# Kernel optimization log

Measured on AMD Instinct MI355X. Metric: run time of the kernel, lower is better.

Reference implementation:

```python
import jax, jax.numpy as jnp
import numpy as np

NUM_HEADS = 4
NUM_EXPERTS = 8
TOP_K = 2
AUX_W = 0.1


def setup_inputs() -> dict:
    key = jax.random.key(0)
    ks = jax.random.split(key, 16)
    B, W, C, T = 32, 64, 27, 2000
    E_EEG, H, S = 200, 256, 768
    D2 = 2 * H  # MoE input/hidden dim = 512
    s = 0.02

    def p(k, shape):
        return (jax.random.normal(k, shape, jnp.float32) * s)

    z = lambda *shape: jnp.zeros(shape, jnp.float32)
    return {
        "eeg_windows": jax.random.normal(ks[0], (B, W, C, T), jnp.float32),
        "padding_mask": jnp.zeros((B, W), bool),
        "smiles_emb": jax.random.normal(ks[1], (B, S), jnp.float32),
        # window encoder (linear stand-in): flatten (C*T) -> E_EEG
        "enc_W": p(ks[2], (C * T, E_EEG)), "enc_b": z(E_EEG),
        # aggregator (masked-mean + linear stand-in): E_EEG -> H
        "agg_W": p(ks[3], (E_EEG, H)), "agg_b": z(H),
        # smiles projection
        "smiles_W": p(ks[4], (S, H)), "smiles_b": z(H),
        # cross attention
        "Wq": p(ks[5], (H, H)), "bq": z(H),
        "Wk": p(ks[6], (H, H)), "bk": z(H),
        "Wv": p(ks[7], (H, H)), "bv": z(H),
        "Wo": p(ks[8], (H, H)), "bo": z(H),
        # MoE gate + experts
        "gate_W": p(ks[9], (D2, NUM_EXPERTS)), "gate_b": z(NUM_EXPERTS),
        "exp_W1": p(ks[10], (NUM_EXPERTS, D2, D2)), "exp_b1": z(NUM_EXPERTS, D2),
        "exp_W2": p(ks[11], (NUM_EXPERTS, D2, H)), "exp_b2": z(NUM_EXPERTS, H),
        # classifier
        "ln_g": jnp.ones((H,), jnp.float32), "ln_b": z(H),
        "cls_W": p(ks[12], (H, 2)), "cls_b": z(2),
    }


def reference(eeg_windows, padding_mask, smiles_emb, enc_W, enc_b, agg_W, agg_b,
              smiles_W, smiles_b, Wq, bq, Wk, bk, Wv, bv, Wo, bo,
              gate_W, gate_b, exp_W1, exp_b1, exp_W2, exp_b2,
              ln_g, ln_b, cls_W, cls_b):
    B, W, C, T = eeg_windows.shape
    H = agg_W.shape[1]
    dh = H // NUM_HEADS

    # --- window encoding (stand-in linear encoder) ---
    wemb = eeg_windows.reshape(B, W, C * T) @ enc_W + enc_b  # (B, W, E_EEG)

    # --- aggregator: masked mean pool over windows, then project ---
    valid = (~padding_mask).astype(wemb.dtype)[..., None]      # (B, W, 1)
    pooled = (wemb * valid).sum(1) / jnp.maximum(valid.sum(1), 1.0)
    eeg_emb = pooled @ agg_W + agg_b                           # (B, H)

    smiles_proj = smiles_emb @ smiles_W + smiles_b             # (B, H)

    # --- cross attention (single query token over single kv token) ---
    q = (eeg_emb @ Wq + bq).reshape(B, NUM_HEADS, dh)
    k = (smiles_proj @ Wk + bk).reshape(B, NUM_HEADS, dh)
    v = (smiles_proj @ Wv + bv).reshape(B, NUM_HEADS, dh)
    scores = (q * k).sum(-1, keepdims=True) / jnp.sqrt(jnp.float32(dh))
    attn = jnp.exp(scores - scores)  # softmax over a single key == 1
    attended = (attn * v).reshape(B, H) @ Wo + bo              # (B, H)

    fused = jnp.concatenate([attended, smiles_proj], axis=-1)  # (B, 2H)

    # --- sparse MoE: dense experts, top-k gate, gather, combine ---
    gate_probs = jax.nn.softmax(fused @ gate_W + gate_b, axis=-1)  # (B, E)
    topk_p, topk_i = jax.lax.top_k(gate_probs, TOP_K)
    topk_p = topk_p / topk_p.sum(-1, keepdims=True)
    h1 = jax.nn.gelu(jnp.einsum('bd,edh->beh', fused, exp_W1) + exp_b1,
                     approximate=False)
    expert_out = jnp.einsum('beh,eho->beo', h1, exp_W2) + exp_b2   # (B, E, H)
    sel = jnp.take_along_axis(expert_out, topk_i[:, :, None], axis=1)
    moe_out = (sel * topk_p[..., None]).sum(1)                     # (B, H)

    usage = gate_probs.mean(0)
    uniform = jnp.ones_like(usage) / usage.shape[-1]
    aux = (usage * jnp.log(uniform) - jnp.log(usage) * uniform).sum()

    # --- classifier: LayerNorm + Linear ---
    mu = moe_out.mean(-1, keepdims=True)
    var = moe_out.var(-1, keepdims=True)
    xn = (moe_out - mu) / jnp.sqrt(var + 1e-5)
    logits = (xn * ln_g + ln_b) @ cls_W + cls_b                    # (B, 2)
    return logits, aux * AUX_W
```

## Files before the change

kernel.cpp:

```cpp
#include <hip/hip_runtime.h>
#include <math.h>

#define HD 256
#define SD 768
#define D2 512
#define NE 8
#define NB 32
#define NBLK 256
#define NTHR 256
#define SFP 516

typedef float f32x4 __attribute__((ext_vector_type(4)));
typedef unsigned u32x4 __attribute__((ext_vector_type(4)));

__device__ __forceinline__ float gelu_exact(float x) {
    return 0.5f * x * (1.0f + erff(x * 0.70710678118654752f));
}

__device__ __forceinline__ void cstf(float* p, float v) {
    __hip_atomic_store(p, v, __ATOMIC_RELAXED, __HIP_MEMORY_SCOPE_AGENT);
}
__device__ __forceinline__ float cldf(const float* p) {
    return __hip_atomic_load(p, __ATOMIC_RELAXED, __HIP_MEMORY_SCOPE_AGENT);
}
__device__ __forceinline__ void csti(int* p, int v) {
    __hip_atomic_store(p, v, __ATOMIC_RELAXED, __HIP_MEMORY_SCOPE_AGENT);
}
__device__ __forceinline__ int cldi(const int* p) {
    return __hip_atomic_load(p, __ATOMIC_RELAXED, __HIP_MEMORY_SCOPE_AGENT);
}

__device__ __forceinline__ void stage16k(const float* __restrict__ gsrc,
                                         float* __restrict__ lds, int t)
{
    const f32x4* src = (const f32x4*)gsrc;
    f32x4 r[16];
    #pragma unroll
    for (int j = 0; j < 16; ++j) {
        const f32x4* p = src + (t + j * 256);
        asm volatile("global_load_dwordx4 %0, %1, off sc0 sc1"
                     : "=v"(r[j]) : "v"(p));
    }
    asm volatile("s_waitcnt vmcnt(0)" ::: "memory");
    __builtin_amdgcn_sched_barrier(0);
    #pragma unroll
    for (int j = 0; j < 16; ++j) {
        int q = t + j * 256;
        *(f32x4*)&lds[(q >> 7) * SFP + (q & 127) * 4] = r[j];
    }
}

__device__ __forceinline__ void post_slot(unsigned* slots, unsigned tok) {
    __syncthreads();
    if (threadIdx.x == 0)
        __hip_atomic_store(slots + blockIdx.x, tok, __ATOMIC_RELAXED,
                           __HIP_MEMORY_SCOPE_AGENT);
}

__device__ __forceinline__ void finish_full(const unsigned* slots,
                                            unsigned* gen, unsigned tok) {
    const int t = threadIdx.x;
    if (blockIdx.x == 0) {
        if (t < 64) {
            const u32x4* p = (const u32x4*)slots + t;
            for (;;) {
                u32x4 v;
                asm volatile("global_load_dwordx4 %0, %1, off sc0 sc1\n\t"
                             "s_waitcnt vmcnt(0)"
                             : "=&v"(v) : "v"(p) : "memory");
                bool ok = (v[0] == tok) & (v[1] == tok) &
                          (v[2] == tok) & (v[3] == tok);
                if (__ballot(ok) == ~0ull) break;
                __builtin_amdgcn_s_sleep(1);
            }
            if (t == 0)
                __hip_atomic_store(gen, tok, __ATOMIC_RELAXED,
                                   __HIP_MEMORY_SCOPE_AGENT);
        }
    } else {
        if (t == 0) {
            while (__hip_atomic_load(gen, __ATOMIC_RELAXED,
                                     __HIP_MEMORY_SCOPE_AGENT) != tok)
                __builtin_amdgcn_s_sleep(1);
        }
    }
    __builtin_amdgcn_fence(__ATOMIC_ACQUIRE, "workgroup");
    __syncthreads();
}

__device__ __forceinline__ void wait_subset(const unsigned* slots, int nq,
                                            unsigned tok) {
    if ((int)threadIdx.x < nq) {
        const u32x4* p = (const u32x4*)slots + threadIdx.x;
        for (;;) {
            u32x4 v;
            asm volatile("global_load_dwordx4 %0, %1, off sc0 sc1\n\t"
                         "s_waitcnt vmcnt(0)"
                         : "=&v"(v) : "v"(p) : "memory");
            if ((v[0] == tok) & (v[1] == tok) & (v[2] == tok) & (v[3] == tok))
                break;
            __builtin_amdgcn_s_sleep(2);
        }
    }
    __builtin_amdgcn_fence(__ATOMIC_ACQUIRE, "workgroup");
    __syncthreads();
}

__device__ __forceinline__ void wait_two_experts(const unsigned* slots,
                                                 int ea, int eb, unsigned tok) {
    if (threadIdx.x < 8) {
        int es = (threadIdx.x < 4) ? ea : eb;
        const u32x4* p = (const u32x4*)slots + es * 4 + (threadIdx.x & 3);
        for (;;) {
            u32x4 v;
            asm volatile("global_load_dwordx4 %0, %1, off sc0 sc1\n\t"
                         "s_waitcnt vmcnt(0)"
                         : "=&v"(v) : "v"(p) : "memory");
            if ((v[0] == tok) & (v[1] == tok) & (v[2] == tok) & (v[3] == tok))
                break;
            __builtin_amdgcn_s_sleep(2);
        }
    }
    __builtin_amdgcn_fence(__ATOMIC_ACQUIRE, "workgroup");
    __syncthreads();
}

#define S_F     0
#define S_W     16512
#define S_R2    (16512 + 8192)
#define S_RED   (16512 + 8192 + 4096)
#define S_SMALL (16512 + 8192 + 4096 + 256)
#define SMEM_F  (16512 + 8192 + 4096 + 256 + 16)

__global__ __launch_bounds__(256) void fused_all(
    const float* __restrict__ smiles,
    const float* __restrict__ sW, const float* __restrict__ sb,
    const float* __restrict__ Wv, const float* __restrict__ bv,
    const float* __restrict__ Wo, const float* __restrict__ bo,
    const float* __restrict__ gW, const float* __restrict__ gb,
    const float* __restrict__ W1, const float* __restrict__ b1,
    const float* __restrict__ W2, const float* __restrict__ b2,
    const float* __restrict__ lng, const float* __restrict__ lnb,
    const float* __restrict__ clsW, const float* __restrict__ clsb,
    float* __restrict__ proj, float* __restrict__ fused,
    float* __restrict__ probs, float* __restrict__ pn,
    int* __restrict__ sel, float* __restrict__ h1,
    float* __restrict__ eo,
    unsigned* __restrict__ slot0, unsigned* __restrict__ slot1,
    unsigned* __restrict__ slot2, unsigned* __restrict__ slot3,
    unsigned* __restrict__ gen, unsigned* __restrict__ LC,
    float* __restrict__ out)
{
    __shared__ __align__(16) float smem[SMEM_F];
    __shared__ unsigned s_lc;
    const int bid = blockIdx.x, t = threadIdx.x;

    if (t == 0)
        s_lc = __hip_atomic_load(LC, __ATOMIC_RELAXED, __HIP_MEMORY_SCOPE_AGENT);
    __syncthreads();
    const unsigned tb = s_lc * 2654435761u;

    {
        int r = bid >> 3, sl = bid & 7;
        float* s_in = smem + S_F;
        float* s_red = smem + S_RED;
        const float* srow = smiles + (size_t)r * SD;
        for (int i = t; i < SD / 4; i += NTHR)
            ((float4*)s_in)[i] = ((const float4*)srow)[i];
        __syncthreads();
        int c = t & 31, kq = t >> 5;
        float acc = 0.f;
        const float* wp = sW + (size_t)(kq * 96) * HD + sl * 32 + c;
        #pragma unroll 8
        for (int k = 0; k < 96; ++k)
            acc = fmaf(s_in[kq * 96 + k], wp[(size_t)k * HD], acc);
        s_red[t] = acc;
        __syncthreads();
        if (t < 32) {
            float s = 0.f;
            #pragma unroll
            for (int q = 0; q < 8; ++q) s += s_red[q * 32 + t];
            int col = sl * 32 + t;
            s += sb[col];
            cstf(proj + r * HD + col, s);
            cstf(fused + (size_t)r * 2 * HD + HD + col, s);
        }
    }
    post_slot(slot0, tb + 1u);

    if (bid < NB) {
        wait_subset(slot0 + bid * 8, 2, tb + 1u);
        int b = bid;
        float* s_p   = smem + S_F;
        float* s_v   = smem + S_F + 256;
        float* s_f2  = smem + S_F + 512;
        float* s_acc = smem + S_R2;
        float* s_red = smem + S_RED;
        float* s_gate = smem + S_SMALL;
        s_p[t] = cldf(proj + b * HD + t);
        __syncthreads();
        int ks = t >> 6, cg = t & 63;

        f32x4 av = {0.f, 0.f, 0.f, 0.f};
        #pragma unroll 16
        for (int kk = 0; kk < 64; ++kk) {
            int k = ks * 64 + kk;
            f32x4 w = *(const f32x4*)(Wv + (size_t)k * HD + cg * 4);
            av += s_p[k] * w;
        }
        *(f32x4*)&s_acc[ks * 256 + cg * 4] = av;
        __syncthreads();
        s_v[t] = s_acc[t] + s_acc[256 + t] + s_acc[512 + t] + s_acc[768 + t]
               + bv[t];
        __syncthreads();

        f32x4 ao = {0.f, 0.f, 0.f, 0.f};
        #pragma unroll 16
        for (int kk = 0; kk < 64; ++kk) {
            int k = ks * 64 + kk;
            f32x4 w = *(const f32x4*)(Wo + (size_t)k * HD + cg * 4);
            ao += s_v[k] * w;
        }
        *(f32x4*)&s_acc[ks * 256 + cg * 4] = ao;
        __syncthreads();
        float att = s_acc[t] + s_acc[256 + t] + s_acc[512 + t] + s_acc[768 + t]
                  + bo[t];
        s_f2[t] = att;
        s_f2[HD + t] = s_p[t];
        cstf(fused + (size_t)b * 2 * HD + t, att);
        __syncthreads();

        int e = t & 7, ch = t >> 3;
        float gp = 0.f;
        #pragma unroll
        for (int j = 0; j < 16; ++j) {
            int d = ch * 16 + j;
            gp = fmaf(s_f2[d], gW[d * NE + e], gp);
        }
        s_red[t] = gp;
        __syncthreads();
        for (int off = 128; off >= 8; off >>= 1) {
            if (t < off) s_red[t] += s_red[t + off];
            __syncthreads();
        }
        if (t < NE) s_gate[t] = s_red[t] + gb[t];
        __syncthreads();
        if (t == 0) {
            float m = s_gate[0];
            for (int i = 1; i < NE; ++i) m = fmaxf(m, s_gate[i]);
            float ex[NE], ssum = 0.f;
            for (int i = 0; i < NE; ++i) { ex[i] = expf(s_gate[i] - m); ssum += ex[i]; }
            float pr[NE];
            for (int i = 0; i < NE; ++i) { pr[i] = ex[i] / ssum; cstf(probs + b * NE + i, pr[i]); }
            int i1 = 0;
            for (int i = 1; i < NE; ++i) if (pr[i] > pr[i1]) i1 = i;
            int i2 = (i1 == 0) ? 1 : 0;
            for (int i = 0; i < NE; ++i) if (i != i1 && pr[i] > pr[i2]) i2 = i;
            float p1 = pr[i1], p2 = pr[i2], s12 = p1 + p2;
            csti(sel + b * 2 + 0, i1);
            csti(sel + b * 2 + 1, i2);
            cstf(pn + b * 2 + 0, p1 / s12);
            cstf(pn + b * 2 + 1, p2 / s12);
        }
    }
    post_slot(slot1, tb + 2u);

    {
        int e = bid >> 5, ct = bid & 31;
        float* s_w = smem + S_W;
        const float* Wb = W1 + (size_t)e * D2 * D2 + ct * 16;
        #pragma unroll
        for (int j = 0; j < 8; ++j) {
            int q = t + j * 256;
            int k = q >> 2, c4 = (q & 3) * 4;
            *(float4*)&s_w[k * 16 + c4] = *(const float4*)(Wb + (size_t)k * D2 + c4);
        }
    }
    finish_full(slot1, gen + 0, tb + 2u);

    {
        int e = bid >> 5, ct = bid & 31;
        float* s_f  = smem + S_F;
        float* s_w  = smem + S_W;
        float* s_r2 = smem + S_R2;
        stage16k(fused, s_f, t);
        __syncthreads();
        int ks = t >> 5, l = t & 31;
        int rg = l >> 2, c4g = l & 3;
        const float* wb = s_w + c4g * 4;
        int k0 = ks * 64;
        f32x4 a0 = {0.f,0.f,0.f,0.f}, a1 = a0, a2 = a0, a3 = a0;
        #pragma unroll 2
        for (int kq = 0; kq < 16; ++kq) {
            int k = k0 + kq * 4;
            f32x4 w0 = *(const f32x4*)&wb[(k + 0) * 16];
            f32x4 w1 = *(const f32x4*)&wb[(k + 1) * 16];
            f32x4 w2 = *(const f32x4*)&wb[(k + 2) * 16];
            f32x4 w3 = *(const f32x4*)&wb[(k + 3) * 16];
            f32x4 f0 = *(const f32x4*)&s_f[(rg     ) * SFP + k];
            f32x4 f1 = *(const f32x4*)&s_f[(rg +  8) * SFP + k];
            f32x4 f2 = *(const f32x4*)&s_f[(rg + 16) * SFP + k];
            f32x4 f3 = *(const f32x4*)&s_f[(rg + 24) * SFP + k];
            a0 += f0[0]*w0 + f0[1]*w1 + f0[2]*w2 + f0[3]*w3;
            a1 += f1[0]*w0 + f1[1]*w1 + f1[2]*w2 + f1[3]*w3;
            a2 += f2[0]*w0 + f2[1]*w1 + f2[2]*w2 + f2[3]*w3;
            a3 += f3[0]*w0 + f3[1]*w1 + f3[2]*w2 + f3[3]*w3;
        }
        *(f32x4*)&s_r2[ks * 512 + (rg     ) * 16 + c4g * 4] = a0;
        *(f32x4*)&s_r2[ks * 512 + (rg +  8) * 16 + c4g * 4] = a1;
        *(f32x4*)&s_r2[ks * 512 + (rg + 16) * 16 + c4g * 4] = a2;
        *(f32x4*)&s_r2[ks * 512 + (rg + 24) * 16 + c4g * 4] = a3;
        __syncthreads();
        #pragma unroll
        for (int o = 0; o < 2; ++o) {
            int outi = t * 2 + o;
            float s = 0.f;
            #pragma unroll
            for (int p = 0; p < 8; ++p) s += s_r2[p * 512 + outi];
            int r = outi >> 4, cl = outi & 15;
            int col = ct * 16 + cl;
            cstf(h1 + ((size_t)e * NB + r) * D2 + col,
                 gelu_exact(s + b1[e * D2 + col]));
        }
    }
    post_slot(slot2, tb + 3u);
    if (bid >= 128) return;

    {
        int e = bid >> 4, ct = bid & 15;
        float* s_w = smem + S_W;
        const float* Wb = W2 + (size_t)e * D2 * HD + ct * 16;
        #pragma unroll
        for (int j = 0; j < 8; ++j) {
            int q = t + j * 256;
            int k = q >> 2, c4 = (q & 3) * 4;
            *(float4*)&s_w[k * 16 + c4] = *(const float4*)(Wb + (size_t)k * HD + c4);
        }
    }
    {
        int e = bid >> 4;
        wait_subset(slot2 + e * 32, 8, tb + 3u);
    }

    {
        int e = bid >> 4, ct = bid & 15;
        float* s_f  = smem + S_F;
        float* s_w  = smem + S_W;
        float* s_r2 = smem + S_R2;
        stage16k(h1 + (size_t)e * NB * D2, s_f, t);
        __syncthreads();
        int ks = t >> 5, l = t & 31;
        int rg = l >> 2, c4g = l & 3;
        const float* wb = s_w + c4g * 4;
        int k0 = ks * 64;
        f32x4 a0 = {0.f,0.f,0.f,0.f}, a1 = a0, a2 = a0, a3 = a0;
        #pragma unroll 2
        for (int kq = 0; kq < 16; ++kq) {
            int k = k0 + kq * 4;
            f32x4 w0 = *(const f32x4*)&wb[(k + 0) * 16];
            f32x4 w1 = *(const f32x4*)&wb[(k + 1) * 16];
            f32x4 w2 = *(const f32x4*)&wb[(k + 2) * 16];
            f32x4 w3 = *(const f32x4*)&wb[(k + 3) * 16];
            f32x4 f0 = *(const f32x4*)&s_f[(rg     ) * SFP + k];
            f32x4 f1 = *(const f32x4*)&s_f[(rg +  8) * SFP + k];
            f32x4 f2 = *(const f32x4*)&s_f[(rg + 16) * SFP + k];
            f32x4 f3 = *(const f32x4*)&s_f[(rg + 24) * SFP + k];
            a0 += f0[0]*w0 + f0[1]*w1 + f0[2]*w2 + f0[3]*w3;
            a1 += f1[0]*w0 + f1[1]*w1 + f1[2]*w2 + f1[3]*w3;
            a2 += f2[0]*w0 + f2[1]*w1 + f2[2]*w2 + f2[3]*w3;
            a3 += f3[0]*w0 + f3[1]*w1 + f3[2]*w2 + f3[3]*w3;
        }
        *(f32x4*)&s_r2[ks * 512 + (rg     ) * 16 + c4g * 4] = a0;
        *(f32x4*)&s_r2[ks * 512 + (rg +  8) * 16 + c4g * 4] = a1;
        *(f32x4*)&s_r2[ks * 512 + (rg + 16) * 16 + c4g * 4] = a2;
        *(f32x4*)&s_r2[ks * 512 + (rg + 24) * 16 + c4g * 4] = a3;
        __syncthreads();
        #pragma unroll
        for (int o = 0; o < 2; ++o) {
            int outi = t * 2 + o;
            float s = 0.f;
            #pragma unroll
            for (int p = 0; p < 8; ++p) s += s_r2[p * 512 + outi];
            int r = outi >> 4, cl = outi & 15;
            int col = ct * 16 + cl;
            cstf(eo + ((size_t)e * NB + r) * HD + col, s + b2[e * HD + col]);
        }
    }
    post_slot(slot3, tb + 4u);
    if (bid >= NB) return;

    {
        int b = bid;
        float* s_red = smem + S_RED;
        float* s_stats = smem + S_SMALL;
        int e0 = cldi(sel + b * 2 + 0), e1 = cldi(sel + b * 2 + 1);
        float p0 = cldf(pn + b * 2 + 0), p1 = cldf(pn + b * 2 + 1);

        wait_two_experts(slot3, e0, e1, tb + 4u);

        float moe = p0 * cldf(eo + ((size_t)e0 * NB + b) * HD + t)
                  + p1 * cldf(eo + ((size_t)e1 * NB + b) * HD + t);

        s_red[t] = moe; __syncthreads();
        for (int off = 128; off > 0; off >>= 1) {
            if (t < off) s_red[t] += s_red[t + off];
            __syncthreads();
        }
        if (t == 0) s_stats[0] = s_red[0] * (1.f / HD);
        __syncthreads();
        float mu = s_stats[0];
        float d = moe - mu;

        s_red[t] = d * d; __syncthreads();
        for (int off = 128; off > 0; off >>= 1) {
            if (t < off) s_red[t] += s_red[t + off];
            __syncthreads();
        }
        if (t == 0) s_stats[1] = s_red[0] * (1.f / HD);
        __syncthreads();

        float xn = d * rsqrtf(s_stats[1] + 1e-5f);
        float y = fmaf(xn, lng[t], lnb[t]);

        s_red[t] = y * clsW[t * 2 + 0]; __syncthreads();
        for (int off = 128; off > 0; off >>= 1) {
            if (t < off) s_red[t] += s_red[t + off];
            __syncthreads();
        }
        if (t == 0) s_stats[2] = s_red[0] + clsb[0];
        __syncthreads();

        s_red[t] = y * clsW[t * 2 + 1]; __syncthreads();
        for (int off = 128; off > 0; off >>= 1) {
            if (t < off) s_red[t] += s_red[t + off];
            __syncthreads();
        }
        if (t == 0) {
            out[b * 2 + 0] = s_stats[2];
            out[b * 2 + 1] = s_red[0] + clsb[1];
        }

        if (bid == 0) {
            __syncthreads();
            s_red[t] = cldf(probs + t);
            __syncthreads();
            for (int off = 128; off >= 8; off >>= 1) {
                if (t < off) s_red[t] += s_red[t + off];
                __syncthreads();
            }
            if (t == 0) {
                float aux = 0.f;
                for (int e = 0; e < NE; ++e) {
                    float u = s_red[e] * (1.f / 32.f);
                    aux += u * logf(0.125f) - logf(u) * 0.125f;
                }
                out[64] = 0.1f * aux;
            }
        }
    }

    if (bid == 0) {
        wait_subset(slot2, 64, tb + 3u);
        if (t == 0)
            __hip_atomic_store(LC, s_lc + 1u, __ATOMIC_RELAXED,
                               __HIP_MEMORY_SCOPE_AGENT);
    }
}

extern "C" void kernel_launch(void* const* d_in, const int* in_sizes, int n_in,
                              void* d_out, int out_size, void* d_ws, size_t ws_size,
                              hipStream_t stream) {
    (void)in_sizes; (void)n_in; (void)out_size; (void)ws_size;
    const float* smiles = (const float*)d_in[2];
    const float* sW  = (const float*)d_in[7];
    const float* sb  = (const float*)d_in[8];
    const float* Wv  = (const float*)d_in[13];
    const float* bv  = (const float*)d_in[14];
    const float* Wo  = (const float*)d_in[15];
    const float* bo  = (const float*)d_in[16];
    const float* gW  = (const float*)d_in[17];
    const float* gb  = (const float*)d_in[18];
    const float* W1  = (const float*)d_in[19];
    const float* b1  = (const float*)d_in[20];
    const float* W2  = (const float*)d_in[21];
    const float* b2  = (const float*)d_in[22];
    const float* lng = (const float*)d_in[23];
    const float* lnb = (const float*)d_in[24];
    const float* cW  = (const float*)d_in[25];
    const float* cb  = (const float*)d_in[26];
    float* out = (float*)d_out;
    float* ws  = (float*)d_ws;

    float*    proj  = ws;
    float*    fused = ws + 8192;
    float*    probs = ws + 24576;
    float*    pn    = ws + 24832;
    int*      sel   = (int*)(ws + 24896);
    float*    h1    = ws + 24960;
    float*    eo    = ws + 156032;
    unsigned* slot0 = (unsigned*)(ws + 221568);
    unsigned* slot1 = (unsigned*)(ws + 221824);
    unsigned* slot2 = (unsigned*)(ws + 222080);
    unsigned* slot3 = (unsigned*)(ws + 222336);
    unsigned* gen   = (unsigned*)(ws + 222592);
    unsigned* LC    = (unsigned*)(ws + 222596);

    fused_all<<<NBLK, NTHR, 0, stream>>>(
        smiles, sW, sb, Wv, bv, Wo, bo, gW, gb, W1, b1, W2, b2,
        lng, lnb, cW, cb,
        proj, fused, probs, pn, sel, h1, eo,
        slot0, slot1, slot2, slot3, gen, LC, out);
}
```

Measured before the change: 37.87 us.

## Precompute fused Wv·Wo matrix across all blocks and use wave-shuffle LayerNorm reductions

All 256 blocks now cooperatively compute the product M = Wv·Wo, plus the folded bias bv·Wo + bo, into workspace during the first stage. The 32 per-batch blocks can then apply a single 256x256 matvec instead of two chained ones. This shortens the serial critical path of those blocks, but every block must now wait on all 64 slot0 entries instead of a small subset. It also adds an extra 256x256x256 GEMM of work. Separately, the LayerNorm/classifier tail replaces shared-memory tree reductions with wavefront shuffle reductions, cutting the number of __syncthreads calls.

```diff
diff --git a/kernel.cpp b/kernel.cpp
--- a/kernel.cpp
+++ b/kernel.cpp
@@ -130,7 +130,7 @@
 #define S_R2    (16512 + 8192)
 #define S_RED   (16512 + 8192 + 4096)
 #define S_SMALL (16512 + 8192 + 4096 + 256)
-#define SMEM_F  (16512 + 8192 + 4096 + 256 + 16)
+#define SMEM_F  (16512 + 8192 + 4096 + 256 + 32)
 
 __global__ __launch_bounds__(256) void fused_all(
     const float* __restrict__ smiles,
@@ -145,7 +145,8 @@
     float* __restrict__ proj, float* __restrict__ fused,
     float* __restrict__ probs, float* __restrict__ pn,
     int* __restrict__ sel, float* __restrict__ h1,
-    float* __restrict__ eo,
+    float* __restrict__ eo, float* __restrict__ Mws,
+    float* __restrict__ attb,
     unsigned* __restrict__ slot0, unsigned* __restrict__ slot1,
     unsigned* __restrict__ slot2, unsigned* __restrict__ slot3,
     unsigned* __restrict__ gen, unsigned* __restrict__ LC,
@@ -186,13 +187,57 @@
             cstf(fused + (size_t)r * 2 * HD + HD + col, s);
         }
     }
+
+    {
+        int ti = bid >> 4, tj = bid & 15;
+        int k0 = ti * 16, c0 = tj * 16;
+        float* sA = smem + S_F;
+        float* sB = smem + S_F + 4160;
+        float* s_red = smem + S_RED;
+        __syncthreads();
+        #pragma unroll
+        for (int j = 0; j < 4; ++j) {
+            int q = t + j * 256;
+            int r = q >> 6, kq4 = q & 63;
+            *(f32x4*)&sA[r * 260 + kq4 * 4] =
+                *(const f32x4*)(Wv + (size_t)(k0 + r) * HD + kq4 * 4);
+        }
+        #pragma unroll
+        for (int j = 0; j < 4; ++j) {
+            int q = t + j * 256;
+            int kk = q >> 2, c4 = q & 3;
+            *(f32x4*)&sB[kk * 16 + c4 * 4] =
+                *(const f32x4*)(Wo + (size_t)kk * HD + c0 + c4 * 4);
+        }
+        __syncthreads();
+        int r = t >> 4, c = t & 15;
+        float acc = 0.f;
+        #pragma unroll 8
+        for (int kk = 0; kk < 256; ++kk)
+            acc = fmaf(sA[r * 260 + kk], sB[kk * 16 + c], acc);
+        cstf(Mws + (size_t)(k0 + r) * HD + c0 + c, acc);
+        if (ti == 0) {
+            int ks2 = t >> 4, c2 = t & 15;
+            float pacc = 0.f;
+            #pragma unroll
+            for (int kk = 0; kk < 16; ++kk)
+                pacc = fmaf(bv[ks2 * 16 + kk], sB[(ks2 * 16 + kk) * 16 + c2], pacc);
+            s_red[t] = pacc;
+            __syncthreads();
+            if (t < 16) {
+                float s = 0.f;
+                #pragma unroll
+                for (int q2 = 0; q2 < 16; ++q2) s += s_red[q2 * 16 + t];
+                cstf(attb + c0 + t, s + bo[c0 + t]);
+            }
+        }
+    }
     post_slot(slot0, tb + 1u);
 
     if (bid < NB) {
-        wait_subset(slot0 + bid * 8, 2, tb + 1u);
+        wait_subset(slot0, 64, tb + 1u);
         int b = bid;
         float* s_p   = smem + S_F;
-        float* s_v   = smem + S_F + 256;
         float* s_f2  = smem + S_F + 512;
         float* s_acc = smem + S_R2;
         float* s_red = smem + S_RED;
@@ -201,30 +246,27 @@
         __syncthreads();
         int ks = t >> 6, cg = t & 63;
 
-        f32x4 av = {0.f, 0.f, 0.f, 0.f};
-        #pragma unroll 16
-        for (int kk = 0; kk < 64; ++kk) {
-            int k = ks * 64 + kk;
-            f32x4 w = *(const f32x4*)(Wv + (size_t)k * HD + cg * 4);
-            av += s_p[k] * w;
-        }
-        *(f32x4*)&s_acc[ks * 256 + cg * 4] = av;
-        __syncthreads();
-        s_v[t] = s_acc[t] + s_acc[256 + t] + s_acc[512 + t] + s_acc[768 + t]
-               + bv[t];
-        __syncthreads();
-
-        f32x4 ao = {0.f, 0.f, 0.f, 0.f};
-        #pragma unroll 16
-        for (int kk = 0; kk < 64; ++kk) {
-            int k = ks * 64 + kk;
-            f32x4 w = *(const f32x4*)(Wo + (size_t)k * HD + cg * 4);
-            ao += s_v[k] * w;
-        }
-        *(f32x4*)&s_acc[ks * 256 + cg * 4] = ao;
+        f32x4 acc4 = {0.f, 0.f, 0.f, 0.f};
+        #pragma unroll
+        for (int rr = 0; rr < 4; ++rr) {
+            f32x4 m[16];
+            #pragma unroll
+            for (int j = 0; j < 16; ++j) {
+                const f32x4* p = (const f32x4*)
+                    (Mws + (size_t)(ks * 64 + rr * 16 + j) * HD + cg * 4);
+                asm volatile("global_load_dwordx4 %0, %1, off sc0 sc1"
+                             : "=v"(m[j]) : "v"(p));
+            }
+            asm volatile("s_waitcnt vmcnt(0)" ::: "memory");
+            __builtin_amdgcn_sched_barrier(0);
+            #pragma unroll
+            for (int j = 0; j < 16; ++j)
+                acc4 += s_p[ks * 64 + rr * 16 + j] * m[j];
+        }
+        *(f32x4*)&s_acc[ks * 256 + cg * 4] = acc4;
         __syncthreads();
         float att = s_acc[t] + s_acc[256 + t] + s_acc[512 + t] + s_acc[768 + t]
-                  + bo[t];
+                  + cldf(attb + t);
         s_f2[t] = att;
         s_f2[HD + t] = s_p[t];
         cstf(fused + (size_t)b * 2 * HD + t, att);
@@ -400,44 +442,38 @@
 
         float moe = p0 * cldf(eo + ((size_t)e0 * NB + b) * HD + t)
                   + p1 * cldf(eo + ((size_t)e1 * NB + b) * HD + t);
-
-        s_red[t] = moe; __syncthreads();
-        for (int off = 128; off > 0; off >>= 1) {
-            if (t < off) s_red[t] += s_red[t + off];
-            __syncthreads();
-        }
-        if (t == 0) s_stats[0] = s_red[0] * (1.f / HD);
-        __syncthreads();
-        float mu = s_stats[0];
+        int wv = t >> 6, ln = t & 63;
+
+        float ssum = moe;
+        #pragma unroll
+        for (int off = 32; off > 0; off >>= 1) ssum += __shfl_down(ssum, off, 64);
+        if (ln == 0) s_stats[4 + wv] = ssum;
+        __syncthreads();
+        float mu = (s_stats[4] + s_stats[5] + s_stats[6] + s_stats[7]) * (1.f / HD);
         float d = moe - mu;
 
-        s_red[t] = d * d; __syncthreads();
-        for (int off = 128; off > 0; off >>= 1) {
-            if (t < off) s_red[t] += s_red[t + off];
-            __syncthreads();
-        }
-        if (t == 0) s_stats[1] = s_red[0] * (1.f / HD);
-        __syncthreads();
-
-        float xn = d * rsqrtf(s_stats[1] + 1e-5f);
-        float y = fmaf(xn, lng[t], lnb[t]);
-
-        s_red[t] = y * clsW[t * 2 + 0]; __syncthreads();
-        for (int off = 128; off > 0; off >>= 1) {
-            if (t < off) s_red[t] += s_red[t + off];
-            __syncthreads();
-        }
-        if (t == 0) s_stats[2] = s_red[0] + clsb[0];
-        __syncthreads();
-
-        s_red[t] = y * clsW[t * 2 + 1]; __syncthreads();
-        for (int off = 128; off > 0; off >>= 1) {
-            if (t < off) s_red[t] += s_red[t + off];
-            __syncthreads();
-        }
+        float vs = d * d;
+        #pragma unroll
+        for (int off = 32; off > 0; off >>= 1) vs += __shfl_down(vs, off, 64);
+        if (ln == 0) s_stats[8 + wv] = vs;
+        __syncthreads();
+        float var = (s_stats[8] + s_stats[9] + s_stats[10] + s_stats[11]) * (1.f / HD);
+
+        float y = fmaf(d * rsqrtf(var + 1e-5f), lng[t], lnb[t]);
+
+        float c0 = y * clsW[t * 2 + 0], c1 = y * clsW[t * 2 + 1];
+        #pragma unroll
+        for (int off = 32; off > 0; off >>= 1) {
+            c0 += __shfl_down(c0, off, 64);
+            c1 += __shfl_down(c1, off, 64);
+        }
+        if (ln == 0) { s_stats[12 + wv] = c0; s_stats[16 + wv] = c1; }
+        __syncthreads();
         if (t == 0) {
-            out[b * 2 + 0] = s_stats[2];
-            out[b * 2 + 1] = s_red[0] + clsb[1];
+            out[b * 2 + 0] = s_stats[12] + s_stats[13] + s_stats[14] + s_stats[15]
+                           + clsb[0];
+            out[b * 2 + 1] = s_stats[16] + s_stats[17] + s_stats[18] + s_stats[19]
+                           + clsb[1];
         }
 
         if (bid == 0) {
@@ -498,16 +534,18 @@
     int*      sel   = (int*)(ws + 24896);
     float*    h1    = ws + 24960;
     float*    eo    = ws + 156032;
+    float*    Mws   = eo;
     unsigned* slot0 = (unsigned*)(ws + 221568);
     unsigned* slot1 = (unsigned*)(ws + 221824);
     unsigned* slot2 = (unsigned*)(ws + 222080);
     unsigned* slot3 = (unsigned*)(ws + 222336);
     unsigned* gen   = (unsigned*)(ws + 222592);
     unsigned* LC    = (unsigned*)(ws + 222596);
+    float*    attb  = ws + 222608;
 
     fused_all<<<NBLK, NTHR, 0, stream>>>(
         smiles, sW, sb, Wv, bv, Wo, bo, gW, gb, W1, b1, W2, b2,
         lng, lnb, cW, cb,
-        proj, fused, probs, pn, sel, h1, eo,
+        proj, fused, probs, pn, sel, h1, eo, Mws, attb,
         slot0, slot1, slot2, slot3, gen, LC, out);
 }
```

Measured after the change: 38.24 us. No clear change (+1.0%).
